# Optimization experiments

Hardware: AMD Instinct MI355X
Metric: run time of the kernel (lower is better)

## Reference

```python
import jax, jax.numpy as jnp
import numpy as np

EPS = 1e-5  # torch BatchNorm2d default


def _conv1x1(x, w):
    # x: [n, cin, h, w], w: [cout, cin] (1x1 conv == per-pixel matmul)
    return jnp.einsum('nchw,oc->nohw', x, w)


def _bn(x, gamma, beta, mean, var):
    # inference-mode BatchNorm2d over channel dim
    scale = gamma * jax.lax.rsqrt(var + EPS)
    shift = beta - mean * scale
    return x * scale[None, :, None, None] + shift[None, :, None, None]


def setup_inputs() -> dict:
    key = jax.random.key(0)
    ks = jax.random.split(key, 24)
    n, c, h, w = 16, 256, 64, 64
    width, planes = c // 2, c
    inp = {
        'x': jax.random.normal(ks[0], (n, c, h, w), jnp.float32),
        'w_theta': jax.random.normal(ks[1], (width, c), jnp.float32) * 0.05,
        'w_phi': jax.random.normal(ks[2], (width, c), jnp.float32) * 0.05,
        'w_g': jax.random.normal(ks[3], (width, c), jnp.float32) * 0.05,
        'w_zeta': jax.random.normal(ks[4], (planes, width), jnp.float32) * 0.05,
    }
    for i, (name, dim) in enumerate([('bn1', width), ('bn2', width), ('bn3', width), ('bn4', planes)]):
        k = 5 + 4 * i
        inp[f'{name}_gamma'] = jax.random.uniform(ks[k], (dim,), jnp.float32, 0.5, 1.5)
        inp[f'{name}_beta'] = jax.random.normal(ks[k + 1], (dim,), jnp.float32) * 0.1
        inp[f'{name}_mean'] = jax.random.normal(ks[k + 2], (dim,), jnp.float32) * 0.1
        inp[f'{name}_var'] = jax.random.uniform(ks[k + 3], (dim,), jnp.float32, 0.5, 1.5)
    return inp


def reference(x, w_theta, w_phi, w_g, w_zeta,
              bn1_gamma, bn1_beta, bn1_mean, bn1_var,
              bn2_gamma, bn2_beta, bn2_mean, bn2_var,
              bn3_gamma, bn3_beta, bn3_mean, bn3_var,
              bn4_gamma, bn4_beta, bn4_mean, bn4_var):
    n, c, h, w = x.shape
    theta = jax.nn.relu(_bn(_conv1x1(x, w_theta), bn1_gamma, bn1_beta, bn1_mean, bn1_var))
    phi = jax.nn.relu(_bn(_conv1x1(x, w_phi), bn2_gamma, bn2_beta, bn2_mean, bn2_var))
    g = jax.nn.relu(_bn(_conv1x1(x, w_g), bn3_gamma, bn3_beta, bn3_mean, bn3_var))

    width = theta.shape[1]
    hw = h * w
    theta = theta.reshape(n, width, hw)  # [n, C', S]
    phi = phi.reshape(n, width, hw)      # [n, C', S]
    g = g.reshape(n, width, hw)          # [n, C', S]

    # (theta^T @ phi) @ g^T == theta^T @ (phi @ g^T): no softmax, so associativity
    # lets us contract over pixels first -> O(S*C'^2) instead of O(S^2*C').
    kv = jnp.einsum('ncs,nds->ncd', phi, g)      # [n, C', C']
    out = jnp.einsum('ncs,ncd->nsd', theta, kv)  # [n, S, C']

    # faithful to torch: reshape (not transpose) [n, S, C'] -> [n, C', h, w]
    out = out.reshape(n, width, h, w)
    out = _bn(_conv1x1(out, w_zeta), bn4_gamma, bn4_beta, bn4_mean, bn4_var)
    return jax.nn.relu(out + x)
```

## Files before the change

### kernel.cpp

```cpp
#include <hip/hip_runtime.h>

#define BN_EPS 1e-5f

typedef unsigned short u16;
typedef __bf16 bf16x8 __attribute__((ext_vector_type(8)));
typedef float floatx4 __attribute__((ext_vector_type(4)));
typedef u16 u16x4 __attribute__((ext_vector_type(4)));
typedef u16 u16x8 __attribute__((ext_vector_type(8)));

__device__ __forceinline__ u16 f2bf(float f) {
    union { float f; unsigned int u; } v; v.f = f;
    unsigned int r = (v.u + 0x7fffu + ((v.u >> 16) & 1u)) >> 16;
    return (u16)r;
}

__device__ __forceinline__ unsigned int cvtpk(float lo, float hi) {
    unsigned int r;
    asm("v_cvt_pk_bf16_f32 %0, %1, %2" : "=v"(r) : "v"(lo), "v"(hi));
    return r;
}

__device__ __forceinline__ void gld16(const void* gsrc, void* ldst) {
    __builtin_amdgcn_global_load_lds(
        (const __attribute__((address_space(1))) unsigned int*)gsrc,
        (__attribute__((address_space(3))) unsigned int*)ldst, 16, 0, 0);
}

__device__ __forceinline__ int addsw(int seg, int s) {
    return (seg + (s & 7) + ((s >> 3) & 7)) & 7;
}

__global__ __launch_bounds__(256) void prep_kernel(
    const float* __restrict__ wt, const float* __restrict__ wp,
    const float* __restrict__ wg, const float* __restrict__ wz,
    const float* __restrict__ g1, const float* __restrict__ b1,
    const float* __restrict__ m1, const float* __restrict__ v1,
    const float* __restrict__ g2, const float* __restrict__ b2,
    const float* __restrict__ m2, const float* __restrict__ v2,
    const float* __restrict__ g3, const float* __restrict__ b3,
    const float* __restrict__ m3, const float* __restrict__ v3,
    const float* __restrict__ g4, const float* __restrict__ b4,
    const float* __restrict__ m4, const float* __restrict__ v4,
    u16* __restrict__ W1bf, float* __restrict__ shift1,
    u16* __restrict__ Wzbf, float* __restrict__ shift4)
{
    int id = blockIdx.x * 256 + threadIdx.x;
    if (id < 384 * 256) {
        int r = id >> 8, c = id & 255;
        int grp = r >> 7, ch = r & 127;
        const float* wsrc = grp == 0 ? wt : (grp == 1 ? wp : wg);
        const float* gg = grp == 0 ? g1 : (grp == 1 ? g2 : g3);
        const float* bb = grp == 0 ? b1 : (grp == 1 ? b2 : b3);
        const float* mm = grp == 0 ? m1 : (grp == 1 ? m2 : m3);
        const float* vv = grp == 0 ? v1 : (grp == 1 ? v2 : v3);
        float scale = gg[ch] * rsqrtf(vv[ch] + BN_EPS);
        W1bf[id] = f2bf(wsrc[ch * 256 + c] * scale);
        if (c == 0) shift1[r] = bb[ch] - mm[ch] * scale;
    }
    if (id < 256 * 128) {
        int o = id >> 7;
        float scale = g4[o] * rsqrtf(v4[o] + BN_EPS);
        Wzbf[id] = f2bf(wz[id] * scale);
        if ((id & 127) == 0) shift4[o] = b4[o] - m4[o] * scale;
    }
}

__global__ __launch_bounds__(512, 2) void k1_kernel(
    const float* __restrict__ x, const u16* __restrict__ W1,
    const float* __restrict__ shift1,
    u16* __restrict__ theta_sm, float* __restrict__ partials)
{
    const int sk = blockIdx.x, n = blockIdx.y;
    const int tid = threadIdx.x;
    const int w = tid >> 6, lane = tid & 63;
    const int quad = lane >> 4, l16 = lane & 15;

    __shared__ __align__(16) u16 ldsA[384 * 64];
    __shared__ __align__(16) u16 ldsB[128 * 64];
    __shared__ __align__(16) u16 ldsPG[4][128 * 64];

    floatx4 kv[8];
#pragma unroll
    for (int i = 0; i < 8; ++i) kv[i] = floatx4{0.f, 0.f, 0.f, 0.f};

    const int cp = w * 4 + quad;
    unsigned int* ldsBdw = (unsigned int*)ldsB;

    float4 xva[2][2], xvb[2][2];

    for (int ss = 0; ss < 2; ++ss) {
        const float* xb = x + ((size_t)n * 256 + 2 * cp) * 4096 + sk * 256 + ss * 128;

        floatx4 acc[3][8];
#pragma unroll
        for (int i = 0; i < 3; ++i)
#pragma unroll
            for (int j = 0; j < 8; ++j) acc[i][j] = floatx4{0.f, 0.f, 0.f, 0.f};

        auto loadx = [&](float4 (&xv)[2][2], int kc) {
#pragma unroll
            for (int ch = 0; ch < 2; ++ch)
#pragma unroll
                for (int hb = 0; hb < 2; ++hb)
                    xv[ch][hb] = *((const float4*)(xb + (size_t)(kc * 64 + ch) * 4096) + hb * 16 + l16);
        };
        auto writeB = [&](const float4 (&xv)[2][2]) {
#pragma unroll
            for (int hb = 0; hb < 2; ++hb)
#pragma unroll
                for (int j = 0; j < 4; ++j) {
                    int s = hb * 64 + l16 * 4 + j;
                    ldsBdw[s * 32 + addsw(w, s) * 4 + quad] =
                        cvtpk(((const float*)&xv[0][hb])[j], ((const float*)&xv[1][hb])[j]);
                }
        };
        auto stageA = [&](int kc) {
#pragma unroll
            for (int i = 0; i < 6; ++i) {
                int op = w * 6 + i;
                int r = op * 8 + (lane >> 3);
                int lseg = (lane & 7) ^ (r & 7);
                gld16(W1 + (size_t)r * 256 + kc * 64 + lseg * 8, ldsA + op * 512);
            }
        };

        loadx(xva, 0);
        for (int kc = 0; kc < 4; ++kc) {
            writeB((kc & 1) ? xvb : xva);
            stageA(kc);
            if (kc < 3) loadx((kc & 1) ? xva : xvb, kc + 1);
            __syncthreads();
#pragma unroll
            for (int kk = 0; kk < 2; ++kk) {
                bf16x8 a[3];
#pragma unroll
                for (int mt = 0; mt < 3; ++mt) {
                    int r = mt * 128 + w * 16 + l16;
                    int phys = (kk * 4 + quad) ^ (r & 7);
                    a[mt] = *(const bf16x8*)(ldsA + r * 64 + phys * 8);
                }
#pragma unroll
                for (int ni = 0; ni < 8; ++ni) {
                    int s = ni * 16 + l16;
                    int phys = addsw(kk * 4 + quad, s);
                    bf16x8 b = *(const bf16x8*)(ldsB + s * 64 + phys * 8);
#pragma unroll
                    for (int mt = 0; mt < 3; ++mt)
                        acc[mt][ni] = __builtin_amdgcn_mfma_f32_16x16x32_bf16(
                            a[mt], b, acc[mt][ni], 0, 0, 0);
                }
            }
            __syncthreads();
        }

        const int ocq = w * 16 + quad * 4;
        {
            float sh0 = shift1[ocq + 0], sh1 = shift1[ocq + 1];
            float sh2 = shift1[ocq + 2], sh3 = shift1[ocq + 3];
#pragma unroll
            for (int ni = 0; ni < 8; ++ni) {
                int s = sk * 256 + ss * 128 + ni * 16 + l16;
                float v0 = acc[0][ni][0] + sh0, v1 = acc[0][ni][1] + sh1;
                float v2 = acc[0][ni][2] + sh2, v3 = acc[0][ni][3] + sh3;
                v0 = v0 > 0.f ? v0 : 0.f;
                v1 = v1 > 0.f ? v1 : 0.f;
                v2 = v2 > 0.f ? v2 : 0.f;
                v3 = v3 > 0.f ? v3 : 0.f;
                uint2 pk;
                pk.x = cvtpk(v0, v1);
                pk.y = cvtpk(v2, v3);
                *(uint2*)(theta_sm + (size_t)n * 524288 + (size_t)s * 128 + ocq) = pk;
            }
        }
#pragma unroll
        for (int mt = 1; mt < 3; ++mt)
#pragma unroll
            for (int r = 0; r < 4; ++r) {
                int ch = ocq + r;
                float sh = shift1[mt * 128 + ch];
#pragma unroll
                for (int ni = 0; ni < 8; ++ni) {
                    int sl = ni * 16 + l16;
                    int half = sl >> 6, s6 = sl & 63;
                    int phys = (s6 >> 3) ^ (ch & 7);
                    float val = acc[mt][ni][r] + sh;
                    val = val > 0.f ? val : 0.f;
                    ldsPG[(mt - 1) * 2 + half][ch * 64 + phys * 8 + (s6 & 7)] = f2bf(val);
                }
            }
        __syncthreads();

#pragma unroll
        for (int h = 0; h < 2; ++h)
#pragma unroll
            for (int kk = 0; kk < 2; ++kk) {
                int rd = w * 16 + l16;
                int physa = (kk * 4 + quad) ^ (rd & 7);
                bf16x8 a = *(const bf16x8*)(ldsPG[2 + h] + rd * 64 + physa * 8);
#pragma unroll
                for (int ci = 0; ci < 8; ++ci) {
                    int rc = ci * 16 + l16;
                    int physb = (kk * 4 + quad) ^ (rc & 7);
                    bf16x8 b = *(const bf16x8*)(ldsPG[h] + rc * 64 + physb * 8);
                    kv[ci] = __builtin_amdgcn_mfma_f32_16x16x32_bf16(a, b, kv[ci], 0, 0, 0);
                }
            }
        __syncthreads();
    }

    float* outp = partials + (size_t)(n * 16 + sk) * 16384;
#pragma unroll
    for (int r = 0; r < 4; ++r) {
        int d = w * 16 + quad * 4 + r;
#pragma unroll
        for (int ci = 0; ci < 8; ++ci)
            outp[d * 128 + ci * 16 + l16] = kv[ci][r];
    }
}

__global__ __launch_bounds__(256) void kv_reduce_kernel(
    const float* __restrict__ partials, u16* __restrict__ kvT)
{
    int n = blockIdx.y;
    int f4 = blockIdx.x * 256 + threadIdx.x;
    const float4* p4 = (const float4*)partials;
    float4 s = {0.f, 0.f, 0.f, 0.f};
#pragma unroll
    for (int kc = 0; kc < 16; ++kc) {
        float4 v = p4[(size_t)(n * 16 + kc) * 4096 + f4];
        s.x += v.x; s.y += v.y; s.z += v.z; s.w += v.w;
    }
    u16x4 o; o[0] = f2bf(s.x); o[1] = f2bf(s.y); o[2] = f2bf(s.z); o[3] = f2bf(s.w);
    *(u16x4*)(kvT + (size_t)n * 16384 + f4 * 4) = o;
}

__global__ __launch_bounds__(512, 2) void k34_kernel(
    const u16* __restrict__ theta_sm, const u16* __restrict__ kvT,
    const u16* __restrict__ Wz, const float* __restrict__ shift4,
    const float* __restrict__ x, float* __restrict__ out)
{
    const int st = blockIdx.x, n = blockIdx.y;
    const int tid = threadIdx.x;
    const int w = tid >> 6, lane = tid & 63;
    const int quad = lane >> 4, l16 = lane & 15;

    __shared__ __align__(16) u16 lds[49152];
    u16* T0 = lds;
    u16* K0 = lds + 8192;
    u16* T1 = lds + 16384;
    u16* K1 = lds + 24576;
    u16* Y  = lds + 32768;

    const u16* tbase = theta_sm + (size_t)n * 524288 + (size_t)st * 128;
    const u16* kbase = kvT + (size_t)n * 16384;

    floatx4 acc3[8];
#pragma unroll
    for (int i = 0; i < 8; ++i) acc3[i] = floatx4{0.f, 0.f, 0.f, 0.f};

    auto stageTK = [&](u16* T, u16* K, int ch) {
#pragma unroll
        for (int i = 0; i < 2; ++i) {
            int op = w * 2 + i;
            int r = op * 8 + (lane >> 3);
            int lseg = (lane & 7) ^ (r & 7);
            gld16(tbase + (size_t)r * 4096 + ch * 64 + lseg * 8, T + op * 512);
            gld16(kbase + (size_t)r * 128 + ch * 64 + lseg * 8, K + op * 512);
        }
    };
    auto comp3 = [&](const u16* T, const u16* K) {
#pragma unroll
        for (int kk = 0; kk < 2; ++kk) {
            int rc2 = w * 16 + l16;
            int physa = (kk * 4 + quad) ^ (rc2 & 7);
            bf16x8 a = *(const bf16x8*)(T + rc2 * 64 + physa * 8);
#pragma unroll
            for (int di = 0; di < 8; ++di) {
                int rd = di * 16 + l16;
                int physb = (kk * 4 + quad) ^ (rd & 7);
                bf16x8 b = *(const bf16x8*)(K + rd * 64 + physb * 8);
                acc3[di] = __builtin_amdgcn_mfma_f32_16x16x32_bf16(a, b, acc3[di], 0, 0, 0);
            }
        }
    };

    stageTK(T0, K0, 0);
    __syncthreads();
    stageTK(T1, K1, 1);
    comp3(T0, K0);
    __syncthreads();
    comp3(T1, K1);

#pragma unroll
    for (int di = 0; di < 8; ++di) {
        int j = di * 16 + l16;
#pragma unroll
        for (int r = 0; r < 4; ++r) {
            int c2 = w * 16 + quad * 4 + r;
            int half = c2 >> 6, c64 = c2 & 63;
            int phys = (c64 >> 3) ^ (j & 7);
            Y[half * 8192 + j * 64 + phys * 8 + (c64 & 7)] = f2bf(acc3[di][r]);
        }
    }
#pragma unroll
    for (int i = 0; i < 4; ++i) {
        int op = w * 4 + i;
        int r = op * 8 + (lane >> 3);
        int lseg = (lane & 7) ^ (r & 7);
        gld16(Wz + (size_t)r * 128 + 0 * 64 + lseg * 8, lds + op * 512);
    }
    __syncthreads();

    floatx4 acc4[2][8];
#pragma unroll
    for (int i = 0; i < 2; ++i)
#pragma unroll
        for (int j = 0; j < 8; ++j) acc4[i][j] = floatx4{0.f, 0.f, 0.f, 0.f};

    auto comp4 = [&](const u16* WL, int ch) {
#pragma unroll
        for (int kk = 0; kk < 2; ++kk) {
            bf16x8 a[2];
#pragma unroll
            for (int mi = 0; mi < 2; ++mi) {
                int r = w * 32 + mi * 16 + l16;
                int phys = (kk * 4 + quad) ^ (r & 7);
                a[mi] = *(const bf16x8*)(WL + r * 64 + phys * 8);
            }
#pragma unroll
            for (int ni = 0; ni < 8; ++ni) {
                int s = ni * 16 + l16;
                int phys = (kk * 4 + quad) ^ (s & 7);
                bf16x8 b = *(const bf16x8*)(Y + ch * 8192 + s * 64 + phys * 8);
#pragma unroll
                for (int mi = 0; mi < 2; ++mi)
                    acc4[mi][ni] = __builtin_amdgcn_mfma_f32_16x16x32_bf16(
                        a[mi], b, acc4[mi][ni], 0, 0, 0);
            }
        }
    };

#pragma unroll
    for (int i = 0; i < 4; ++i) {
        int op = w * 4 + i;
        int r = op * 8 + (lane >> 3);
        int lseg = (lane & 7) ^ (r & 7);
        gld16(Wz + (size_t)r * 128 + 1 * 64 + lseg * 8, lds + 16384 + op * 512);
    }
    comp4(lds, 0);
    __syncthreads();
    comp4(lds + 16384, 1);

#pragma unroll
    for (int mi = 0; mi < 2; ++mi)
#pragma unroll
        for (int r = 0; r < 4; ++r) {
            int o = w * 32 + mi * 16 + quad * 4 + r;
            float sh = shift4[o];
#pragma unroll
            for (int ni = 0; ni < 8; ++ni) {
                int s2 = st * 128 + ni * 16 + l16;
                size_t idx = ((size_t)n * 256 + o) * 4096 + s2;
                float val = acc4[mi][ni][r] + sh + x[idx];
                out[idx] = val > 0.f ? val : 0.f;
            }
        }
}

extern "C" void kernel_launch(void* const* d_in, const int* in_sizes, int n_in,
                              void* d_out, int out_size, void* d_ws, size_t ws_size,
                              hipStream_t stream)
{
    const float* x  = (const float*)d_in[0];
    const float* wt = (const float*)d_in[1];
    const float* wp = (const float*)d_in[2];
    const float* wg = (const float*)d_in[3];
    const float* wz = (const float*)d_in[4];
    const float* bn[16];
    for (int i = 0; i < 16; ++i) bn[i] = (const float*)d_in[5 + i];

    char* ws = (char*)d_ws;
    u16*   W1bf     = (u16*)  (ws + 0);
    float* shift1   = (float*)(ws + 196608);
    u16*   Wzbf     = (u16*)  (ws + 198144);
    float* shift4   = (float*)(ws + 263680);
    u16*   theta_sm = (u16*)  (ws + 264704);
    float* partials = (float*)(ws + 17041920);
    u16*   kvT      = (u16*)  (ws + 33819136);
    float* out = (float*)d_out;

    prep_kernel<<<384, 256, 0, stream>>>(
        wt, wp, wg, wz,
        bn[0], bn[1], bn[2], bn[3],
        bn[4], bn[5], bn[6], bn[7],
        bn[8], bn[9], bn[10], bn[11],
        bn[12], bn[13], bn[14], bn[15],
        W1bf, shift1, Wzbf, shift4);

    k1_kernel<<<dim3(16, 16), 512, 0, stream>>>(x, W1bf, shift1, theta_sm, partials);
    kv_reduce_kernel<<<dim3(16, 16), 256, 0, stream>>>(partials, kvT);
    k34_kernel<<<dim3(32, 16), 512, 0, stream>>>(theta_sm, kvT, Wzbf, shift4, x, out);
}
```

Baseline: 221.6 us.

## Split k1 over more pixel blocks and shrink LDS to raise occupancy

k1 now handles 128 pixels per block instead of two 128-pixel passes, so it launches twice as many blocks and writes twice as many kv partials, which the reduce kernel sums over 32 chunks. Both k1 and k34 pack their shared memory into one 64KB pool that is reused across phases, and launch bounds are raised to 4 blocks per CU. k34 now loads the Wz tiles into the freed region after the theta/kv stage. The change trades more partial-sum traffic and extra barriers in k34 for higher occupancy and better latency hiding.

```diff
diff --git a/kernel.cpp b/kernel.cpp
--- a/kernel.cpp
+++ b/kernel.cpp
@@ -65,7 +65,7 @@
     }
 }
 
-__global__ __launch_bounds__(512, 2) void k1_kernel(
+__global__ __launch_bounds__(512, 4) void k1_kernel(
     const float* __restrict__ x, const u16* __restrict__ W1,
     const float* __restrict__ shift1,
     u16* __restrict__ theta_sm, float* __restrict__ partials)
@@ -75,140 +75,135 @@
     const int w = tid >> 6, lane = tid & 63;
     const int quad = lane >> 4, l16 = lane & 15;
 
-    __shared__ __align__(16) u16 ldsA[384 * 64];
-    __shared__ __align__(16) u16 ldsB[128 * 64];
-    __shared__ __align__(16) u16 ldsPG[4][128 * 64];
+    __shared__ __align__(16) u16 pool[32768];
+    u16* ldsA = pool;
+    u16* ldsB = pool + 24576;
+
+    floatx4 acc[3][8];
+#pragma unroll
+    for (int i = 0; i < 3; ++i)
+#pragma unroll
+        for (int j = 0; j < 8; ++j) acc[i][j] = floatx4{0.f, 0.f, 0.f, 0.f};
+
+    const int cp = w * 4 + quad;
+    const float* xb = x + ((size_t)n * 256 + 2 * cp) * 4096 + sk * 128;
+    unsigned int* ldsBdw = (unsigned int*)ldsB;
+
+    float4 xv[2][2];
+
+    auto loadx = [&](int kc) {
+#pragma unroll
+        for (int ch = 0; ch < 2; ++ch)
+#pragma unroll
+            for (int hb = 0; hb < 2; ++hb)
+                xv[ch][hb] = *((const float4*)(xb + (size_t)(kc * 64 + ch) * 4096) + hb * 16 + l16);
+    };
+    auto writeB = [&]() {
+#pragma unroll
+        for (int hb = 0; hb < 2; ++hb)
+#pragma unroll
+            for (int j = 0; j < 4; ++j) {
+                int s = hb * 64 + l16 * 4 + j;
+                ldsBdw[s * 32 + addsw(w, s) * 4 + quad] =
+                    cvtpk(((const float*)&xv[0][hb])[j], ((const float*)&xv[1][hb])[j]);
+            }
+    };
+    auto stageA = [&](int kc) {
+#pragma unroll
+        for (int i = 0; i < 6; ++i) {
+            int op = w * 6 + i;
+            int r = op * 8 + (lane >> 3);
+            int lseg = (lane & 7) ^ (r & 7);
+            gld16(W1 + (size_t)r * 256 + kc * 64 + lseg * 8, ldsA + op * 512);
+        }
+    };
+
+    loadx(0);
+    for (int kc = 0; kc < 4; ++kc) {
+        writeB();
+        if (kc < 3) loadx(kc + 1);
+        stageA(kc);
+        __syncthreads();
+#pragma unroll
+        for (int kk = 0; kk < 2; ++kk) {
+            bf16x8 a[3];
+#pragma unroll
+            for (int mt = 0; mt < 3; ++mt) {
+                int r = mt * 128 + w * 16 + l16;
+                int phys = (kk * 4 + quad) ^ (r & 7);
+                a[mt] = *(const bf16x8*)(ldsA + r * 64 + phys * 8);
+            }
+#pragma unroll
+            for (int ni = 0; ni < 8; ++ni) {
+                int s = ni * 16 + l16;
+                int phys = addsw(kk * 4 + quad, s);
+                bf16x8 b = *(const bf16x8*)(ldsB + s * 64 + phys * 8);
+#pragma unroll
+                for (int mt = 0; mt < 3; ++mt)
+                    acc[mt][ni] = __builtin_amdgcn_mfma_f32_16x16x32_bf16(
+                        a[mt], b, acc[mt][ni], 0, 0, 0);
+            }
+        }
+        __syncthreads();
+    }
+
+    const int ocq = w * 16 + quad * 4;
+    {
+        float sh0 = shift1[ocq + 0], sh1 = shift1[ocq + 1];
+        float sh2 = shift1[ocq + 2], sh3 = shift1[ocq + 3];
+#pragma unroll
+        for (int ni = 0; ni < 8; ++ni) {
+            int s = sk * 128 + ni * 16 + l16;
+            float v0 = acc[0][ni][0] + sh0, v1 = acc[0][ni][1] + sh1;
+            float v2 = acc[0][ni][2] + sh2, v3 = acc[0][ni][3] + sh3;
+            v0 = v0 > 0.f ? v0 : 0.f;
+            v1 = v1 > 0.f ? v1 : 0.f;
+            v2 = v2 > 0.f ? v2 : 0.f;
+            v3 = v3 > 0.f ? v3 : 0.f;
+            uint2 pk;
+            pk.x = cvtpk(v0, v1);
+            pk.y = cvtpk(v2, v3);
+            *(uint2*)(theta_sm + (size_t)n * 524288 + (size_t)s * 128 + ocq) = pk;
+        }
+    }
+#pragma unroll
+    for (int mt = 1; mt < 3; ++mt)
+#pragma unroll
+        for (int r = 0; r < 4; ++r) {
+            int ch = ocq + r;
+            float sh = shift1[mt * 128 + ch];
+#pragma unroll
+            for (int ni = 0; ni < 8; ++ni) {
+                int sl = ni * 16 + l16;
+                int half = sl >> 6, s6 = sl & 63;
+                int phys = (s6 >> 3) ^ (ch & 7);
+                float val = acc[mt][ni][r] + sh;
+                val = val > 0.f ? val : 0.f;
+                pool[((mt - 1) * 2 + half) * 8192 + ch * 64 + phys * 8 + (s6 & 7)] = f2bf(val);
+            }
+        }
+    __syncthreads();
 
     floatx4 kv[8];
 #pragma unroll
     for (int i = 0; i < 8; ++i) kv[i] = floatx4{0.f, 0.f, 0.f, 0.f};
-
-    const int cp = w * 4 + quad;
-    unsigned int* ldsBdw = (unsigned int*)ldsB;
-
-    float4 xva[2][2], xvb[2][2];
-
-    for (int ss = 0; ss < 2; ++ss) {
-        const float* xb = x + ((size_t)n * 256 + 2 * cp) * 4096 + sk * 256 + ss * 128;
-
-        floatx4 acc[3][8];
-#pragma unroll
-        for (int i = 0; i < 3; ++i)
-#pragma unroll
-            for (int j = 0; j < 8; ++j) acc[i][j] = floatx4{0.f, 0.f, 0.f, 0.f};
-
-        auto loadx = [&](float4 (&xv)[2][2], int kc) {
-#pragma unroll
-            for (int ch = 0; ch < 2; ++ch)
-#pragma unroll
-                for (int hb = 0; hb < 2; ++hb)
-                    xv[ch][hb] = *((const float4*)(xb + (size_t)(kc * 64 + ch) * 4096) + hb * 16 + l16);
-        };
-        auto writeB = [&](const float4 (&xv)[2][2]) {
-#pragma unroll
-            for (int hb = 0; hb < 2; ++hb)
-#pragma unroll
-                for (int j = 0; j < 4; ++j) {
-                    int s = hb * 64 + l16 * 4 + j;
-                    ldsBdw[s * 32 + addsw(w, s) * 4 + quad] =
-                        cvtpk(((const float*)&xv[0][hb])[j], ((const float*)&xv[1][hb])[j]);
-                }
-        };
-        auto stageA = [&](int kc) {
-#pragma unroll
-            for (int i = 0; i < 6; ++i) {
-                int op = w * 6 + i;
-                int r = op * 8 + (lane >> 3);
-                int lseg = (lane & 7) ^ (r & 7);
-                gld16(W1 + (size_t)r * 256 + kc * 64 + lseg * 8, ldsA + op * 512);
-            }
-        };
-
-        loadx(xva, 0);
-        for (int kc = 0; kc < 4; ++kc) {
-            writeB((kc & 1) ? xvb : xva);
-            stageA(kc);
-            if (kc < 3) loadx((kc & 1) ? xva : xvb, kc + 1);
-            __syncthreads();
-#pragma unroll
-            for (int kk = 0; kk < 2; ++kk) {
-                bf16x8 a[3];
-#pragma unroll
-                for (int mt = 0; mt < 3; ++mt) {
-                    int r = mt * 128 + w * 16 + l16;
-                    int phys = (kk * 4 + quad) ^ (r & 7);
-                    a[mt] = *(const bf16x8*)(ldsA + r * 64 + phys * 8);
-                }
-#pragma unroll
-                for (int ni = 0; ni < 8; ++ni) {
-                    int s = ni * 16 + l16;
-                    int phys = addsw(kk * 4 + quad, s);
-                    bf16x8 b = *(const bf16x8*)(ldsB + s * 64 + phys * 8);
-#pragma unroll
-                    for (int mt = 0; mt < 3; ++mt)
-                        acc[mt][ni] = __builtin_amdgcn_mfma_f32_16x16x32_bf16(
-                            a[mt], b, acc[mt][ni], 0, 0, 0);
-                }
-            }
-            __syncthreads();
-        }
-
-        const int ocq = w * 16 + quad * 4;
-        {
-            float sh0 = shift1[ocq + 0], sh1 = shift1[ocq + 1];
-            float sh2 = shift1[ocq + 2], sh3 = shift1[ocq + 3];
-#pragma unroll
-            for (int ni = 0; ni < 8; ++ni) {
-                int s = sk * 256 + ss * 128 + ni * 16 + l16;
-                float v0 = acc[0][ni][0] + sh0, v1 = acc[0][ni][1] + sh1;
-                float v2 = acc[0][ni][2] + sh2, v3 = acc[0][ni][3] + sh3;
-                v0 = v0 > 0.f ? v0 : 0.f;
-                v1 = v1 > 0.f ? v1 : 0.f;
-                v2 = v2 > 0.f ? v2 : 0.f;
-                v3 = v3 > 0.f ? v3 : 0.f;
-                uint2 pk;
-                pk.x = cvtpk(v0, v1);
-                pk.y = cvtpk(v2, v3);
-                *(uint2*)(theta_sm + (size_t)n * 524288 + (size_t)s * 128 + ocq) = pk;
-            }
-        }
-#pragma unroll
-        for (int mt = 1; mt < 3; ++mt)
-#pragma unroll
-            for (int r = 0; r < 4; ++r) {
-                int ch = ocq + r;
-                float sh = shift1[mt * 128 + ch];
-#pragma unroll
-                for (int ni = 0; ni < 8; ++ni) {
-                    int sl = ni * 16 + l16;
-                    int half = sl >> 6, s6 = sl & 63;
-                    int phys = (s6 >> 3) ^ (ch & 7);
-                    float val = acc[mt][ni][r] + sh;
-                    val = val > 0.f ? val : 0.f;
-                    ldsPG[(mt - 1) * 2 + half][ch * 64 + phys * 8 + (s6 & 7)] = f2bf(val);
-                }
-            }
-        __syncthreads();
-
-#pragma unroll
-        for (int h = 0; h < 2; ++h)
-#pragma unroll
-            for (int kk = 0; kk < 2; ++kk) {
-                int rd = w * 16 + l16;
-                int physa = (kk * 4 + quad) ^ (rd & 7);
-                bf16x8 a = *(const bf16x8*)(ldsPG[2 + h] + rd * 64 + physa * 8);
-#pragma unroll
-                for (int ci = 0; ci < 8; ++ci) {
-                    int rc = ci * 16 + l16;
-                    int physb = (kk * 4 + quad) ^ (rc & 7);
-                    bf16x8 b = *(const bf16x8*)(ldsPG[h] + rc * 64 + physb * 8);
-                    kv[ci] = __builtin_amdgcn_mfma_f32_16x16x32_bf16(a, b, kv[ci], 0, 0, 0);
-                }
-            }
-        __syncthreads();
-    }
-
-    float* outp = partials + (size_t)(n * 16 + sk) * 16384;
+#pragma unroll
+    for (int h = 0; h < 2; ++h)
+#pragma unroll
+        for (int kk = 0; kk < 2; ++kk) {
+            int rd = w * 16 + l16;
+            int physa = (kk * 4 + quad) ^ (rd & 7);
+            bf16x8 a = *(const bf16x8*)(pool + (2 + h) * 8192 + rd * 64 + physa * 8);
+#pragma unroll
+            for (int ci = 0; ci < 8; ++ci) {
+                int rc = ci * 16 + l16;
+                int physb = (kk * 4 + quad) ^ (rc & 7);
+                bf16x8 b = *(const bf16x8*)(pool + h * 8192 + rc * 64 + physb * 8);
+                kv[ci] = __builtin_amdgcn_mfma_f32_16x16x32_bf16(a, b, kv[ci], 0, 0, 0);
+            }
+        }
+
+    float* outp = partials + (size_t)(n * 32 + sk) * 16384;
 #pragma unroll
     for (int r = 0; r < 4; ++r) {
         int d = w * 16 + quad * 4 + r;
@@ -226,15 +221,15 @@
     const float4* p4 = (const float4*)partials;
     float4 s = {0.f, 0.f, 0.f, 0.f};
 #pragma unroll
-    for (int kc = 0; kc < 16; ++kc) {
-        float4 v = p4[(size_t)(n * 16 + kc) * 4096 + f4];
+    for (int kc = 0; kc < 32; ++kc) {
+        float4 v = p4[(size_t)(n * 32 + kc) * 4096 + f4];
         s.x += v.x; s.y += v.y; s.z += v.z; s.w += v.w;
     }
     u16x4 o; o[0] = f2bf(s.x); o[1] = f2bf(s.y); o[2] = f2bf(s.z); o[3] = f2bf(s.w);
     *(u16x4*)(kvT + (size_t)n * 16384 + f4 * 4) = o;
 }
 
-__global__ __launch_bounds__(512, 2) void k34_kernel(
+__global__ __launch_bounds__(512, 4) void k34_kernel(
     const u16* __restrict__ theta_sm, const u16* __restrict__ kvT,
     const u16* __restrict__ Wz, const float* __restrict__ shift4,
     const float* __restrict__ x, float* __restrict__ out)
@@ -244,12 +239,8 @@
     const int w = tid >> 6, lane = tid & 63;
     const int quad = lane >> 4, l16 = lane & 15;
 
-    __shared__ __align__(16) u16 lds[49152];
-    u16* T0 = lds;
-    u16* K0 = lds + 8192;
-    u16* T1 = lds + 16384;
-    u16* K1 = lds + 24576;
-    u16* Y  = lds + 32768;
+    __shared__ __align__(16) u16 pool[32768];
+    u16* Y = pool + 16384;
 
     const u16* tbase = theta_sm + (size_t)n * 524288 + (size_t)st * 128;
     const u16* kbase = kvT + (size_t)n * 16384;
@@ -268,6 +259,15 @@
             gld16(kbase + (size_t)r * 128 + ch * 64 + lseg * 8, K + op * 512);
         }
     };
+    auto stageWz = [&](int ch) {
+#pragma unroll
+        for (int i = 0; i < 4; ++i) {
+            int op = w * 4 + i;
+            int r = op * 8 + (lane >> 3);
+            int lseg = (lane & 7) ^ (r & 7);
+            gld16(Wz + (size_t)r * 128 + ch * 64 + lseg * 8, pool + op * 512);
+        }
+    };
     auto comp3 = [&](const u16* T, const u16* K) {
 #pragma unroll
         for (int kk = 0; kk < 2; ++kk) {
@@ -284,12 +284,14 @@
         }
     };
 
-    stageTK(T0, K0, 0);
-    __syncthreads();
-    stageTK(T1, K1, 1);
-    comp3(T0, K0);
-    __syncthreads();
-    comp3(T1, K1);
+    stageTK(pool, pool + 8192, 0);
+    __syncthreads();
+    stageTK(pool + 16384, pool + 24576, 1);
+    comp3(pool, pool + 8192);
+    __syncthreads();
+    stageWz(0);
+    comp3(pool + 16384, pool + 24576);
+    __syncthreads();
 
 #pragma unroll
     for (int di = 0; di < 8; ++di) {
@@ -302,13 +304,6 @@
             Y[half * 8192 + j * 64 + phys * 8 + (c64 & 7)] = f2bf(acc3[di][r]);
         }
     }
-#pragma unroll
-    for (int i = 0; i < 4; ++i) {
-        int op = w * 4 + i;
-        int r = op * 8 + (lane >> 3);
-        int lseg = (lane & 7) ^ (r & 7);
-        gld16(Wz + (size_t)r * 128 + 0 * 64 + lseg * 8, lds + op * 512);
-    }
     __syncthreads();
 
     floatx4 acc4[2][8];
@@ -317,7 +312,7 @@
 #pragma unroll
         for (int j = 0; j < 8; ++j) acc4[i][j] = floatx4{0.f, 0.f, 0.f, 0.f};
 
-    auto comp4 = [&](const u16* WL, int ch) {
+    auto comp4 = [&](int ch) {
 #pragma unroll
         for (int kk = 0; kk < 2; ++kk) {
             bf16x8 a[2];
@@ -325,7 +320,7 @@
             for (int mi = 0; mi < 2; ++mi) {
                 int r = w * 32 + mi * 16 + l16;
                 int phys = (kk * 4 + quad) ^ (r & 7);
-                a[mi] = *(const bf16x8*)(WL + r * 64 + phys * 8);
+                a[mi] = *(const bf16x8*)(pool + r * 64 + phys * 8);
             }
 #pragma unroll
             for (int ni = 0; ni < 8; ++ni) {
@@ -340,16 +335,11 @@
         }
     };
 
-#pragma unroll
-    for (int i = 0; i < 4; ++i) {
-        int op = w * 4 + i;
-        int r = op * 8 + (lane >> 3);
-        int lseg = (lane & 7) ^ (r & 7);
-        gld16(Wz + (size_t)r * 128 + 1 * 64 + lseg * 8, lds + 16384 + op * 512);
-    }
-    comp4(lds, 0);
-    __syncthreads();
-    comp4(lds + 16384, 1);
+    comp4(0);
+    __syncthreads();
+    stageWz(1);
+    __syncthreads();
+    comp4(1);
 
 #pragma unroll
     for (int mi = 0; mi < 2; ++mi)
@@ -386,7 +376,7 @@
     float* shift4   = (float*)(ws + 263680);
     u16*   theta_sm = (u16*)  (ws + 264704);
     float* partials = (float*)(ws + 17041920);
-    u16*   kvT      = (u16*)  (ws + 33819136);
+    u16*   kvT      = (u16*)  (ws + 50596352);
     float* out = (float*)d_out;
 
     prep_kernel<<<384, 256, 0, stream>>>(
@@ -397,7 +387,7 @@
         bn[12], bn[13], bn[14], bn[15],
         W1bf, shift1, Wzbf, shift4);
 
-    k1_kernel<<<dim3(16, 16), 512, 0, stream>>>(x, W1bf, shift1, theta_sm, partials);
+    k1_kernel<<<dim3(32, 16), 512, 0, stream>>>(x, W1bf, shift1, theta_sm, partials);
     kv_reduce_kernel<<<dim3(16, 16), 256, 0, stream>>>(partials, kvT);
     k34_kernel<<<dim3(32, 16), 512, 0, stream>>>(theta_sm, kvT, Wzbf, shift4, x, out);
 }
```

Measured after the change: 314.4 us. +41.9%, slower.
